# Kernel optimization log

Hardware: AMD Instinct MI355X
Metric: run time of the kernel (lower is better)

## Reference

```python
import jax, jax.numpy as jnp
import numpy as np

FEAT = 1152
HID = [768, 512, 256]
WS = 32
LN_EPS = 1e-5


def _ln(x, g, b):
    mu = jnp.mean(x, axis=-1, keepdims=True)
    var = jnp.mean(jnp.square(x - mu), axis=-1, keepdims=True)
    return (x - mu) * jax.lax.rsqrt(var + LN_EPS) * g + b


def setup_inputs() -> dict:
    key = jax.random.key(0)
    ks = jax.random.split(key, 16)
    B, N, C = 8, 9216, FEAT

    def lin(k, din, dout):
        s = 1.0 / np.sqrt(din)
        k1, k2 = jax.random.split(k)
        return (jax.random.uniform(k1, (din, dout), jnp.float32, -s, s),
                jax.random.uniform(k2, (dout,), jnp.float32, -s, s))

    x = jax.random.normal(ks[0], (B, N, C), jnp.float32)
    W1, b1 = lin(ks[1], C, HID[0])
    W2, b2 = lin(ks[2], HID[0], HID[1])
    W3, b3 = lin(ks[3], HID[1], HID[2])
    Wo, bo = lin(ks[4], HID[2], C)
    red = C // 8
    ca_w1, ca_b1 = lin(ks[5], C, red)
    ca_w2, ca_b2 = lin(ks[6], red, C)
    return {
        "x": x,
        "W1": W1, "b1": b1, "g1": jnp.ones((HID[0],)), "be1": jnp.zeros((HID[0],)),
        "W2": W2, "b2": b2, "g2": jnp.ones((HID[1],)), "be2": jnp.zeros((HID[1],)),
        "W3": W3, "b3": b3, "g3": jnp.ones((HID[2],)), "be3": jnp.zeros((HID[2],)),
        "Wo": Wo, "bo": bo,
        "ca_w1": ca_w1, "ca_b1": ca_b1, "ca_w2": ca_w2, "ca_b2": ca_b2,
    }


def reference(x, W1, b1, g1, be1, W2, b2, g2, be2, W3, b3, g3, be3,
              Wo, bo, ca_w1, ca_b1, ca_w2, ca_b2):
    B, N, C = x.shape
    # projection + hidden blocks: Linear -> GELU(exact) -> LayerNorm
    h = _ln(jax.nn.gelu(x @ W1 + b1, approximate=False), g1, be1)
    h = _ln(jax.nn.gelu(h @ W2 + b2, approximate=False), g2, be2)
    h = _ln(jax.nn.gelu(h @ W3 + b3, approximate=False), g3, be3)
    y = h @ Wo + bo  # (B, N, C)
    # SE channel attention: global avg-pool over seq, 1x1 convs (=linear)
    pooled = jnp.mean(y, axis=1)                                  # (B, C)
    s = jax.nn.relu(pooled @ ca_w1 + ca_b1)                       # (B, C/8)
    s = jax.nn.sigmoid(s @ ca_w2 + ca_b2)                         # (B, C)
    y = y * s[:, None, :]
    # block-diagonal local self-attention, window = WS, scale 1/sqrt(C)
    nw = N // WS
    yw = y.reshape(B, nw, WS, C)
    scores = jnp.einsum('bwqc,bwkc->bwqk', yw, yw) / jnp.sqrt(jnp.asarray(C, y.dtype))
    attn = jax.nn.softmax(scores, axis=-1)
    out = jnp.einsum('bwqk,bwkc->bwqc', attn, yw)
    return out.reshape(B, N, C)
```

## Files before the change

### kernel.cpp

```cpp
#include <hip/hip_runtime.h>
#include <cstdint>
#include <cstddef>

typedef __bf16 bf16;
typedef __bf16 bf16x8 __attribute__((ext_vector_type(8)));
typedef float f32x4 __attribute__((ext_vector_type(4)));

__device__ __forceinline__ void gload_lds16(const bf16* g, bf16* l) {
    __builtin_amdgcn_global_load_lds((const __attribute__((address_space(1))) void*)g,
                                     (__attribute__((address_space(3))) void*)l, 16, 0, 0);
}

__global__ void cvt_f32_bf16_kernel(const float* __restrict__ in, bf16* __restrict__ outp, size_t n) {
    const size_t i = ((size_t)blockIdx.x * 256 + threadIdx.x) * 8;
    if (i >= n) return;
    const float4 a = *(const float4*)(in + i);
    const float4 b = *(const float4*)(in + i + 4);
    bf16x8 o;
    o[0] = (bf16)a.x; o[1] = (bf16)a.y; o[2] = (bf16)a.z; o[3] = (bf16)a.w;
    o[4] = (bf16)b.x; o[5] = (bf16)b.y; o[6] = (bf16)b.z; o[7] = (bf16)b.w;
    *(bf16x8*)(outp + i) = o;
}

__global__ void wtrans_all_kernel(const float* __restrict__ W1, bf16* __restrict__ T1,
                                  const float* __restrict__ W2, bf16* __restrict__ T2,
                                  const float* __restrict__ W3, bf16* __restrict__ T3,
                                  const float* __restrict__ Wo, bf16* __restrict__ To)
{
    __shared__ bf16 tile[64][65];
    const int id = blockIdx.x;
    const int t = threadIdx.x;
    const float* W; bf16* T; int K, N, kb, nb;
    if (id < 216)      { W = W1; T = T1; K = 1152; N = 768;  const int r = id;       kb = r % 18; nb = r / 18; }
    else if (id < 312) { W = W2; T = T2; K = 768;  N = 512;  const int r = id - 216; kb = r % 12; nb = r / 12; }
    else if (id < 344) { W = W3; T = T3; K = 512;  N = 256;  const int r = id - 312; kb = r % 8;  nb = r / 8;  }
    else               { W = Wo; T = To; K = 256;  N = 1152; const int r = id - 344; kb = r % 4;  nb = r / 4;  }
    const int k0 = kb << 6;
    const int n0 = nb << 6;
#pragma unroll
    for (int i = 0; i < 16; ++i) {
        const int flat = i * 256 + t;
        const int r = flat >> 6;
        const int c = flat & 63;
        tile[c][r] = (bf16)W[(size_t)(k0 + r) * N + n0 + c];
    }
    __syncthreads();
#pragma unroll
    for (int i = 0; i < 16; ++i) {
        const int flat = i * 256 + t;
        const int r = flat >> 6;
        const int c = flat & 63;
        T[(size_t)(n0 + r) * K + k0 + c] = tile[r][c];
    }
}

__device__ __forceinline__ int xcd_swz(int bid, int nwg) {
    return (bid & 7) * (nwg >> 3) + (bid >> 3);
}

__global__ void gemm_bf16_kernel(const bf16* __restrict__ A, const bf16* __restrict__ Bt,
                                 const float* __restrict__ bias, bf16* __restrict__ C,
                                 int K, int N, int nx, int do_gelu)
{
    __shared__ bf16 Alds[128 * 64];
    __shared__ bf16 Blds[128 * 64];
    const int t = threadIdx.x;
    const int w = t >> 6;
    const int l = t & 63;
    const int l15 = l & 15, l4 = l >> 4;
    const int wgid = xcd_swz(blockIdx.x, gridDim.x);
    const int mblk = wgid / nx;
    const int nblk = wgid - mblk * nx;
    const int m0 = mblk << 7;
    const int n0 = nblk << 7;
    const int wm = (w >> 1) << 6;
    const int wn = (w & 1) << 6;

    f32x4 acc[4][4] = {};

    int sr[4], sg[4];
#pragma unroll
    for (int i = 0; i < 4; ++i) {
        const int flat = i * 256 + t;
        sr[i] = flat >> 3;
        sg[i] = ((flat & 7) ^ (sr[i] & 7)) << 3;
    }

    for (int k0 = 0; k0 < K; k0 += 64) {
#pragma unroll
        for (int i = 0; i < 4; ++i) {
            gload_lds16(A + (size_t)(m0 + sr[i]) * K + (k0 + sg[i]),
                        &Alds[(size_t)(i * 256 + (w << 6)) << 3]);
            gload_lds16(Bt + (size_t)(n0 + sr[i]) * K + (k0 + sg[i]),
                        &Blds[(size_t)(i * 256 + (w << 6)) << 3]);
        }
        __syncthreads();
#pragma unroll
        for (int kk = 0; kk < 2; ++kk) {
            bf16x8 af[4], bfv[4];
#pragma unroll
            for (int i = 0; i < 4; ++i) {
                const int r = wm + (i << 4) + l15;
                const int g = (kk << 2) + l4;
                af[i] = *(const bf16x8*)&Alds[(r << 6) + ((g ^ (r & 7)) << 3)];
                const int rn = wn + (i << 4) + l15;
                bfv[i] = *(const bf16x8*)&Blds[(rn << 6) + ((g ^ (rn & 7)) << 3)];
            }
#pragma unroll
            for (int i = 0; i < 4; ++i)
#pragma unroll
                for (int j = 0; j < 4; ++j)
                    acc[i][j] = __builtin_amdgcn_mfma_f32_16x16x32_bf16(af[i], bfv[j], acc[i][j], 0, 0, 0);
        }
        __syncthreads();
    }

#pragma unroll
    for (int i = 0; i < 4; ++i) {
        const int mb = m0 + wm + (i << 4) + (l4 << 2);
#pragma unroll
        for (int j = 0; j < 4; ++j) {
            const int col = n0 + wn + (j << 4) + l15;
            const float bv = bias[col];
#pragma unroll
            for (int r = 0; r < 4; ++r) {
                float v = acc[i][j][r] + bv;
                if (do_gelu) v = 0.5f * v * (1.0f + erff(v * 0.70710678118654752f));
                C[(size_t)(mb + r) * N + col] = (bf16)v;
            }
        }
    }
}

__global__ void ln768_kernel(bf16* __restrict__ H, const float* __restrict__ g,
                             const float* __restrict__ be)
{
    const int t = threadIdx.x;
    const int rloc = t >> 7;
    const int u = t & 127;
    bf16* hp = H + ((size_t)blockIdx.x * 2 + rloc) * 768;
    float v[8];
    float s1 = 0.f, s2 = 0.f;
    if (u < 96) {
        const bf16x8 hv = *(const bf16x8*)(hp + u * 8);
#pragma unroll
        for (int e = 0; e < 8; ++e) { v[e] = (float)hv[e]; s1 += v[e]; s2 += v[e] * v[e]; }
    }
#pragma unroll
    for (int m = 1; m < 64; m <<= 1) { s1 += __shfl_xor(s1, m, 64); s2 += __shfl_xor(s2, m, 64); }
    __shared__ float red[8];
    const int w = t >> 6;
    if ((t & 63) == 0) { red[w] = s1; red[w + 4] = s2; }
    __syncthreads();
    const int wb = rloc << 1;
    s1 = red[wb] + red[wb + 1];
    s2 = red[wb + 4] + red[wb + 5];
    const float mu = s1 * (1.0f / 768.0f);
    const float rstd = rsqrtf(s2 * (1.0f / 768.0f) - mu * mu + 1e-5f);
    if (u < 96) {
        const float4 g0 = *(const float4*)(g + u * 8);
        const float4 g1 = *(const float4*)(g + u * 8 + 4);
        const float4 b0 = *(const float4*)(be + u * 8);
        const float4 b1 = *(const float4*)(be + u * 8 + 4);
        bf16x8 o;
        o[0] = (bf16)((v[0] - mu) * rstd * g0.x + b0.x);
        o[1] = (bf16)((v[1] - mu) * rstd * g0.y + b0.y);
        o[2] = (bf16)((v[2] - mu) * rstd * g0.z + b0.z);
        o[3] = (bf16)((v[3] - mu) * rstd * g0.w + b0.w);
        o[4] = (bf16)((v[4] - mu) * rstd * g1.x + b1.x);
        o[5] = (bf16)((v[5] - mu) * rstd * g1.y + b1.y);
        o[6] = (bf16)((v[6] - mu) * rstd * g1.z + b1.z);
        o[7] = (bf16)((v[7] - mu) * rstd * g1.w + b1.w);
        *(bf16x8*)(hp + u * 8) = o;
    }
}

__global__ void ln512_kernel(bf16* __restrict__ H, const float* __restrict__ g,
                             const float* __restrict__ be)
{
    const int t = threadIdx.x;
    const int w = t >> 6, l = t & 63;
    bf16* hp = H + ((size_t)blockIdx.x * 4 + w) * 512;
    const bf16x8 hv = *(const bf16x8*)(hp + l * 8);
    float v[8];
    float s1 = 0.f, s2 = 0.f;
#pragma unroll
    for (int e = 0; e < 8; ++e) { v[e] = (float)hv[e]; s1 += v[e]; s2 += v[e] * v[e]; }
#pragma unroll
    for (int m = 1; m < 64; m <<= 1) { s1 += __shfl_xor(s1, m, 64); s2 += __shfl_xor(s2, m, 64); }
    const float mu = s1 * (1.0f / 512.0f);
    const float rstd = rsqrtf(s2 * (1.0f / 512.0f) - mu * mu + 1e-5f);
    const float4 g0 = *(const float4*)(g + l * 8);
    const float4 g1 = *(const float4*)(g + l * 8 + 4);
    const float4 b0 = *(const float4*)(be + l * 8);
    const float4 b1 = *(const float4*)(be + l * 8 + 4);
    bf16x8 o;
    o[0] = (bf16)((v[0] - mu) * rstd * g0.x + b0.x);
    o[1] = (bf16)((v[1] - mu) * rstd * g0.y + b0.y);
    o[2] = (bf16)((v[2] - mu) * rstd * g0.z + b0.z);
    o[3] = (bf16)((v[3] - mu) * rstd * g0.w + b0.w);
    o[4] = (bf16)((v[4] - mu) * rstd * g1.x + b1.x);
    o[5] = (bf16)((v[5] - mu) * rstd * g1.y + b1.y);
    o[6] = (bf16)((v[6] - mu) * rstd * g1.z + b1.z);
    o[7] = (bf16)((v[7] - mu) * rstd * g1.w + b1.w);
    *(bf16x8*)(hp + l * 8) = o;
}

__global__ void ln256_kernel(bf16* __restrict__ H, const float* __restrict__ g,
                             const float* __restrict__ be)
{
    const int t = threadIdx.x;
    const int rloc = t >> 5, l = t & 31;
    bf16* hp = H + ((size_t)blockIdx.x * 8 + rloc) * 256;
    const bf16x8 hv = *(const bf16x8*)(hp + l * 8);
    float v[8];
    float s1 = 0.f, s2 = 0.f;
#pragma unroll
    for (int e = 0; e < 8; ++e) { v[e] = (float)hv[e]; s1 += v[e]; s2 += v[e] * v[e]; }
#pragma unroll
    for (int m = 1; m < 32; m <<= 1) { s1 += __shfl_xor(s1, m, 64); s2 += __shfl_xor(s2, m, 64); }
    const float mu = s1 * (1.0f / 256.0f);
    const float rstd = rsqrtf(s2 * (1.0f / 256.0f) - mu * mu + 1e-5f);
    const float4 g0 = *(const float4*)(g + l * 8);
    const float4 g1 = *(const float4*)(g + l * 8 + 4);
    const float4 b0 = *(const float4*)(be + l * 8);
    const float4 b1 = *(const float4*)(be + l * 8 + 4);
    bf16x8 o;
    o[0] = (bf16)((v[0] - mu) * rstd * g0.x + b0.x);
    o[1] = (bf16)((v[1] - mu) * rstd * g0.y + b0.y);
    o[2] = (bf16)((v[2] - mu) * rstd * g0.z + b0.z);
    o[3] = (bf16)((v[3] - mu) * rstd * g0.w + b0.w);
    o[4] = (bf16)((v[4] - mu) * rstd * g1.x + b1.x);
    o[5] = (bf16)((v[5] - mu) * rstd * g1.y + b1.y);
    o[6] = (bf16)((v[6] - mu) * rstd * g1.z + b1.z);
    o[7] = (bf16)((v[7] - mu) * rstd * g1.w + b1.w);
    *(bf16x8*)(hp + l * 8) = o;
}

__global__ void pool1_kernel(const bf16* __restrict__ Y, float* __restrict__ ppart) {
    const int c = blockIdx.x * 128 + threadIdx.x;
    const int nc = blockIdx.y;
    const int b = blockIdx.z;
    const bf16* yp = Y + ((size_t)b * 9216 + (size_t)nc * 256) * 1152 + c;
    float s = 0.f;
#pragma unroll 4
    for (int i = 0; i < 256; ++i) s += (float)yp[(size_t)i * 1152];
    ppart[((size_t)b * 36 + nc) * 1152 + c] = s;
}

__global__ void se_kernel(const float* __restrict__ ppart,
                          const float* __restrict__ w1, const float* __restrict__ b1,
                          const float* __restrict__ w2, const float* __restrict__ b2,
                          float* __restrict__ sbuf)
{
    const int b = blockIdx.x, t = threadIdx.x;
    __shared__ float p[1152];
    __shared__ float t1[144];
    for (int c = t; c < 1152; c += 256) {
        float s = 0.f;
#pragma unroll
        for (int j = 0; j < 36; ++j) s += ppart[((size_t)b * 36 + j) * 1152 + c];
        p[c] = s * (1.0f / 9216.0f);
    }
    __syncthreads();
    if (t < 144) {
        float a = b1[t];
        for (int k = 0; k < 1152; ++k) a += p[k] * w1[k * 144 + t];
        t1[t] = a > 0.f ? a : 0.f;
    }
    __syncthreads();
    for (int c = t; c < 1152; c += 256) {
        float a = b2[c];
#pragma unroll 8
        for (int k = 0; k < 144; ++k) a += t1[k] * w2[k * 1152 + c];
        sbuf[b * 1152 + c] = 1.0f / (1.0f + expf(-a));
    }
}

__device__ __forceinline__ int fswz(int r) { return (r & 7) ^ ((r >> 3) & 3); }

__global__ void attn_kernel(const bf16* __restrict__ Y, const float* __restrict__ sbuf,
                            float* __restrict__ out)
{
    __shared__ bf16 yw[32 * 384];
    __shared__ float Sp[4][32][33];
    __shared__ bf16 P[32 * 32];

    const int t = threadIdx.x;
    const int w = t >> 6, l = t & 63;
    const int l15 = l & 15, l4 = l >> 4;
    const int wdx = blockIdx.x, b = blockIdx.y;

    const bf16* Yp = Y + ((size_t)b * 9216 + (size_t)wdx * 32) * 1152;
    const float* sv = sbuf + b * 1152;
    float* op = out + ((size_t)b * 9216 + (size_t)wdx * 32) * 1152;

    auto stage_chunk = [&](int cc) {
#pragma unroll
        for (int i = 0; i < 6; ++i) {
            const int flat = i * 256 + t;
            const int r = flat / 48;
            const int gg = flat - r * 48;
            const int c0 = cc * 384 + gg * 8;
            const bf16x8 yv = *(const bf16x8*)(Yp + (size_t)r * 1152 + c0);
            const float4 sa = *(const float4*)(sv + c0);
            const float4 sb = *(const float4*)(sv + c0 + 4);
            bf16x8 ov;
            ov[0] = (bf16)((float)yv[0] * sa.x);
            ov[1] = (bf16)((float)yv[1] * sa.y);
            ov[2] = (bf16)((float)yv[2] * sa.z);
            ov[3] = (bf16)((float)yv[3] * sa.w);
            ov[4] = (bf16)((float)yv[4] * sb.x);
            ov[5] = (bf16)((float)yv[5] * sb.y);
            ov[6] = (bf16)((float)yv[6] * sb.z);
            ov[7] = (bf16)((float)yv[7] * sb.w);
            *(bf16x8*)&yw[((r * 48) + (gg ^ fswz(r))) << 3] = ov;
        }
    };

    f32x4 acc[2][2] = {};
    for (int cc = 0; cc < 3; ++cc) {
        if (cc) __syncthreads();
        stage_chunk(cc);
        __syncthreads();
#pragma unroll
        for (int kkl = 0; kkl < 3; ++kkl) {
            const int g = ((w * 3 + kkl) << 2) + l4;
            bf16x8 af[2];
#pragma unroll
            for (int i = 0; i < 2; ++i) {
                const int r = (i << 4) + l15;
                af[i] = *(const bf16x8*)&yw[((r * 48) + (g ^ fswz(r))) << 3];
            }
#pragma unroll
            for (int i = 0; i < 2; ++i)
#pragma unroll
                for (int j = 0; j < 2; ++j)
                    acc[i][j] = __builtin_amdgcn_mfma_f32_16x16x32_bf16(af[i], af[j], acc[i][j], 0, 0, 0);
        }
    }
#pragma unroll
    for (int i = 0; i < 2; ++i)
#pragma unroll
        for (int j = 0; j < 2; ++j)
#pragma unroll
            for (int r = 0; r < 4; ++r)
                Sp[w][(i << 4) + (l4 << 2) + r][(j << 4) + l15] = acc[i][j][r];
    __syncthreads();

    {
        const int q = t >> 3, u = t & 7;
        float v[4];
#pragma unroll
        for (int e = 0; e < 4; ++e) {
            const int k2 = (u << 2) + e;
            v[e] = (Sp[0][q][k2] + Sp[1][q][k2] + Sp[2][q][k2] + Sp[3][q][k2]) * 0.029462782549439483f;
        }
        float mx = fmaxf(fmaxf(v[0], v[1]), fmaxf(v[2], v[3]));
#pragma unroll
        for (int m = 1; m < 8; m <<= 1) mx = fmaxf(mx, __shfl_xor(mx, m, 64));
        float sm = 0.f;
#pragma unroll
        for (int e = 0; e < 4; ++e) { v[e] = expf(v[e] - mx); sm += v[e]; }
#pragma unroll
        for (int m = 1; m < 8; m <<= 1) sm += __shfl_xor(sm, m, 64);
        const float inv = 1.0f / sm;
#pragma unroll
        for (int e = 0; e < 4; ++e) P[(q << 5) + (u << 2) + e] = (bf16)(v[e] * inv);
    }
    __syncthreads();

    bf16x8 pa[2];
#pragma unroll
    for (int i = 0; i < 2; ++i)
        pa[i] = *(const bf16x8*)&P[(((i << 4) + l15) << 5) + (l4 << 3)];

    for (int ci = 0; ci < 3; ++ci) {
        const int cc = (ci == 0) ? 2 : (ci - 1);
        if (ci) {
            __syncthreads();
            stage_chunk(cc);
            __syncthreads();
        }
        f32x4 pacc[2][6] = {};
#pragma unroll
        for (int jn = 0; jn < 6; ++jn) {
            const int nl = w * 96 + (jn << 4) + l15;
            const int gg = nl >> 3, e = nl & 7;
            bf16x8 bv;
#pragma unroll
            for (int j = 0; j < 8; ++j) {
                const int kr = (l4 << 3) + j;
                bv[j] = yw[(((kr * 48) + (gg ^ fswz(kr))) << 3) + e];
            }
#pragma unroll
            for (int i = 0; i < 2; ++i)
                pacc[i][jn] = __builtin_amdgcn_mfma_f32_16x16x32_bf16(pa[i], bv, pacc[i][jn], 0, 0, 0);
        }
#pragma unroll
        for (int i = 0; i < 2; ++i) {
            const int mb = (i << 4) + (l4 << 2);
#pragma unroll
            for (int jn = 0; jn < 6; ++jn) {
                const int cg = cc * 384 + w * 96 + (jn << 4) + l15;
#pragma unroll
                for (int r = 0; r < 4; ++r)
                    op[(size_t)(mb + r) * 1152 + cg] = pacc[i][jn][r];
            }
        }
    }
}

extern "C" void kernel_launch(void* const* d_in, const int* in_sizes, int n_in,
                              void* d_out, int out_size, void* d_ws, size_t ws_size,
                              hipStream_t stream)
{
    const float* x   = (const float*)d_in[0];
    const float* W1  = (const float*)d_in[1];
    const float* b1  = (const float*)d_in[2];
    const float* g1  = (const float*)d_in[3];
    const float* be1 = (const float*)d_in[4];
    const float* W2  = (const float*)d_in[5];
    const float* b2  = (const float*)d_in[6];
    const float* g2  = (const float*)d_in[7];
    const float* be2 = (const float*)d_in[8];
    const float* W3  = (const float*)d_in[9];
    const float* b3  = (const float*)d_in[10];
    const float* g3  = (const float*)d_in[11];
    const float* be3 = (const float*)d_in[12];
    const float* Wo  = (const float*)d_in[13];
    const float* bo  = (const float*)d_in[14];
    const float* cw1 = (const float*)d_in[15];
    const float* cb1 = (const float*)d_in[16];
    const float* cw2 = (const float*)d_in[17];
    const float* cb2 = (const float*)d_in[18];
    float* out = (float*)d_out;

    const int M = 8 * 9216;
    size_t off = 0;
    auto alloc = [&](size_t nbytes) {
        void* p = (char*)d_ws + off;
        off += (nbytes + 255) & ~(size_t)255;
        return p;
    };
    bf16* Yb  = (bf16*)alloc((size_t)M * 1152 * 2);
    bf16* Hb  = (bf16*)alloc((size_t)M * 768 * 2);
    bf16* H2  = (bf16*)alloc((size_t)M * 512 * 2);
    bf16* Wt1 = (bf16*)alloc(768ull * 1152 * 2);
    bf16* Wt2 = (bf16*)alloc(512ull * 768 * 2);
    bf16* Wt3 = (bf16*)alloc(256ull * 512 * 2);
    bf16* Wto = (bf16*)alloc(1152ull * 256 * 2);
    float* ppart = (float*)alloc(8ull * 36 * 1152 * 4);
    float* sbuf  = (float*)alloc(8ull * 1152 * 4);
    bf16* Xb = Yb;
    bf16* H1 = Hb;
    bf16* H3 = Hb;

    cvt_f32_bf16_kernel<<<41472, 256, 0, stream>>>(x, Xb, (size_t)M * 1152);
    wtrans_all_kernel<<<416, 256, 0, stream>>>(W1, Wt1, W2, Wt2, W3, Wt3, Wo, Wto);

    gemm_bf16_kernel<<<6 * 576, 256, 0, stream>>>(Xb, Wt1, b1, H1, 1152, 768, 6, 1);
    ln768_kernel<<<M / 2, 256, 0, stream>>>(H1, g1, be1);
    gemm_bf16_kernel<<<4 * 576, 256, 0, stream>>>(H1, Wt2, b2, H2, 768, 512, 4, 1);
    ln512_kernel<<<M / 4, 256, 0, stream>>>(H2, g2, be2);
    gemm_bf16_kernel<<<2 * 576, 256, 0, stream>>>(H2, Wt3, b3, H3, 512, 256, 2, 1);
    ln256_kernel<<<M / 8, 256, 0, stream>>>(H3, g3, be3);
    gemm_bf16_kernel<<<9 * 576, 256, 0, stream>>>(H3, Wto, bo, Yb, 256, 1152, 9, 0);

    pool1_kernel<<<dim3(9, 36, 8), 128, 0, stream>>>(Yb, ppart);
    se_kernel<<<8, 256, 0, stream>>>(ppart, cw1, cb1, cw2, cb2, sbuf);
    attn_kernel<<<dim3(288, 8), 256, 0, stream>>>(Yb, sbuf, out);
}
```

Before: 871.6 us.

## Replace GEMM with 256x128-tile, 512-thread, triple-buffered LDS pipelined kernel

The bf16 GEMM changes from 128x128 tiles with 256 threads to 256x128 tiles with 512 threads (8 waves). The K loop now triple-buffers LDS tiles, prefetching two steps ahead with global_load_lds, and interleaves those prefetches with MFMA groups under s_setprio. Synchronisation uses explicit vmcnt waits plus a single barrier per K step. The aim is to hide global-load latency and cut barrier stalls, in exchange for more LDS use (144KB per block), which limits occupancy.

```diff
diff --git a/kernel.cpp b/kernel.cpp
--- a/kernel.cpp
+++ b/kernel.cpp
@@ -58,69 +58,143 @@
     return (bid & 7) * (nwg >> 3) + (bid >> 3);
 }
 
-__global__ void gemm_bf16_kernel(const bf16* __restrict__ A, const bf16* __restrict__ Bt,
-                                 const float* __restrict__ bias, bf16* __restrict__ C,
-                                 int K, int N, int nx, int do_gelu)
-{
-    __shared__ bf16 Alds[128 * 64];
-    __shared__ bf16 Blds[128 * 64];
+__global__ __launch_bounds__(512, 2)
+void gemm_dp_kernel(const bf16* __restrict__ A, const bf16* __restrict__ Bt,
+                    const float* __restrict__ bias, bf16* __restrict__ C,
+                    int K, int N, int nx, int do_gelu)
+{
+    __shared__ bf16 lds[3 * 24576];
     const int t = threadIdx.x;
-    const int w = t >> 6;
-    const int l = t & 63;
+    const int w = t >> 6, l = t & 63;
     const int l15 = l & 15, l4 = l >> 4;
     const int wgid = xcd_swz(blockIdx.x, gridDim.x);
-    const int mblk = wgid / nx;
-    const int nblk = wgid - mblk * nx;
-    const int m0 = mblk << 7;
+    const int mblk = wgid / nx, nblk = wgid - mblk * nx;
+    const int m0 = mblk << 8;
     const int n0 = nblk << 7;
-    const int wm = (w >> 1) << 6;
-    const int wn = (w & 1) << 6;
+    const int wmB = (w >> 1) << 6;
+    const int wnB = (w & 1) << 6;
 
     f32x4 acc[4][4] = {};
 
-    int sr[4], sg[4];
+    int aRow[4], aCol[4];
 #pragma unroll
     for (int i = 0; i < 4; ++i) {
-        const int flat = i * 256 + t;
-        sr[i] = flat >> 3;
-        sg[i] = ((flat & 7) ^ (sr[i] & 7)) << 3;
-    }
-
-    for (int k0 = 0; k0 < K; k0 += 64) {
-#pragma unroll
-        for (int i = 0; i < 4; ++i) {
-            gload_lds16(A + (size_t)(m0 + sr[i]) * K + (k0 + sg[i]),
-                        &Alds[(size_t)(i * 256 + (w << 6)) << 3]);
-            gload_lds16(Bt + (size_t)(n0 + sr[i]) * K + (k0 + sg[i]),
-                        &Blds[(size_t)(i * 256 + (w << 6)) << 3]);
-        }
-        __syncthreads();
-#pragma unroll
-        for (int kk = 0; kk < 2; ++kk) {
-            bf16x8 af[4], bfv[4];
-#pragma unroll
-            for (int i = 0; i < 4; ++i) {
-                const int r = wm + (i << 4) + l15;
-                const int g = (kk << 2) + l4;
-                af[i] = *(const bf16x8*)&Alds[(r << 6) + ((g ^ (r & 7)) << 3)];
-                const int rn = wn + (i << 4) + l15;
-                bfv[i] = *(const bf16x8*)&Blds[(rn << 6) + ((g ^ (rn & 7)) << 3)];
-            }
-#pragma unroll
-            for (int i = 0; i < 4; ++i)
-#pragma unroll
-                for (int j = 0; j < 4; ++j)
-                    acc[i][j] = __builtin_amdgcn_mfma_f32_16x16x32_bf16(af[i], bfv[j], acc[i][j], 0, 0, 0);
-        }
-        __syncthreads();
+        const int flat = i * 512 + t;
+        aRow[i] = flat >> 3;
+        aCol[i] = ((flat & 7) ^ (aRow[i] & 7)) << 3;
+    }
+
+    const int NT = K >> 6;
+
+    auto stageA2 = [&](int kt, int ps, int i0) {
+#pragma unroll
+        for (int i2 = 0; i2 < 2; ++i2) {
+            const int i = i0 + i2;
+            gload_lds16(A + (size_t)(m0 + aRow[i]) * K + (kt << 6) + aCol[i],
+                        &lds[ps * 24576 + ((i * 512 + (w << 6)) << 3)]);
+        }
+    };
+    auto stageB2 = [&](int kt, int ps) {
+#pragma unroll
+        for (int i = 0; i < 2; ++i) {
+            gload_lds16(Bt + (size_t)(n0 + aRow[i]) * K + (kt << 6) + aCol[i],
+                        &lds[ps * 24576 + 16384 + ((i * 512 + (w << 6)) << 3)]);
+        }
+    };
+
+    stageA2(0, 0, 0); stageA2(0, 0, 2); stageB2(0, 0);
+    stageA2(1, 1, 0); stageA2(1, 1, 2); stageB2(1, 1);
+    asm volatile("s_waitcnt vmcnt(6)" ::: "memory");
+    __builtin_amdgcn_s_barrier();
+
+    int s = 0;
+    for (int kt = 0; kt < NT; ++kt) {
+        const int ps = (s == 0) ? 2 : s - 1;
+        const bool pf = (kt + 2) < NT;
+        const bf16* lA = &lds[s * 24576];
+        const bf16* lB = &lds[s * 24576 + 16384];
+
+        bf16x8 bfr[4], afr[2];
+
+#pragma unroll
+        for (int n = 0; n < 4; ++n) {
+            const int r = wnB + (n << 4) + l15;
+            bfr[n] = *(const bf16x8*)&lB[(r << 6) + ((l4 ^ (r & 7)) << 3)];
+        }
+#pragma unroll
+        for (int mi = 0; mi < 2; ++mi) {
+            const int r = wmB + (mi << 4) + l15;
+            afr[mi] = *(const bf16x8*)&lA[(r << 6) + ((l4 ^ (r & 7)) << 3)];
+        }
+        if (pf) stageA2(kt + 2, ps, 0);
+        __builtin_amdgcn_s_setprio(1);
+#pragma unroll
+        for (int mi = 0; mi < 2; ++mi)
+#pragma unroll
+            for (int n = 0; n < 4; ++n)
+                acc[mi][n] = __builtin_amdgcn_mfma_f32_16x16x32_bf16(afr[mi], bfr[n], acc[mi][n], 0, 0, 0);
+        __builtin_amdgcn_s_setprio(0);
+
+#pragma unroll
+        for (int mi = 0; mi < 2; ++mi) {
+            const int r = wmB + ((mi + 2) << 4) + l15;
+            afr[mi] = *(const bf16x8*)&lA[(r << 6) + ((l4 ^ (r & 7)) << 3)];
+        }
+        if (pf) stageA2(kt + 2, ps, 2);
+        __builtin_amdgcn_s_setprio(1);
+#pragma unroll
+        for (int mi = 0; mi < 2; ++mi)
+#pragma unroll
+            for (int n = 0; n < 4; ++n)
+                acc[mi + 2][n] = __builtin_amdgcn_mfma_f32_16x16x32_bf16(afr[mi], bfr[n], acc[mi + 2][n], 0, 0, 0);
+        __builtin_amdgcn_s_setprio(0);
+
+#pragma unroll
+        for (int n = 0; n < 4; ++n) {
+            const int r = wnB + (n << 4) + l15;
+            bfr[n] = *(const bf16x8*)&lB[(r << 6) + (((4 + l4) ^ (r & 7)) << 3)];
+        }
+#pragma unroll
+        for (int mi = 0; mi < 2; ++mi) {
+            const int r = wmB + (mi << 4) + l15;
+            afr[mi] = *(const bf16x8*)&lA[(r << 6) + (((4 + l4) ^ (r & 7)) << 3)];
+        }
+        if (pf) stageB2(kt + 2, ps);
+        __builtin_amdgcn_s_setprio(1);
+#pragma unroll
+        for (int mi = 0; mi < 2; ++mi)
+#pragma unroll
+            for (int n = 0; n < 4; ++n)
+                acc[mi][n] = __builtin_amdgcn_mfma_f32_16x16x32_bf16(afr[mi], bfr[n], acc[mi][n], 0, 0, 0);
+        __builtin_amdgcn_s_setprio(0);
+
+#pragma unroll
+        for (int mi = 0; mi < 2; ++mi) {
+            const int r = wmB + ((mi + 2) << 4) + l15;
+            afr[mi] = *(const bf16x8*)&lA[(r << 6) + (((4 + l4) ^ (r & 7)) << 3)];
+        }
+        __builtin_amdgcn_s_setprio(1);
+#pragma unroll
+        for (int mi = 0; mi < 2; ++mi)
+#pragma unroll
+            for (int n = 0; n < 4; ++n)
+                acc[mi + 2][n] = __builtin_amdgcn_mfma_f32_16x16x32_bf16(afr[mi], bfr[n], acc[mi + 2][n], 0, 0, 0);
+        __builtin_amdgcn_s_setprio(0);
+
+        if (kt + 1 < NT) {
+            if (pf) { asm volatile("s_waitcnt vmcnt(6)" ::: "memory"); }
+            else    { asm volatile("s_waitcnt vmcnt(0)" ::: "memory"); }
+            __builtin_amdgcn_s_barrier();
+        }
+        s = (s == 2) ? 0 : s + 1;
     }
 
 #pragma unroll
     for (int i = 0; i < 4; ++i) {
-        const int mb = m0 + wm + (i << 4) + (l4 << 2);
+        const int mb = m0 + wmB + (i << 4) + (l4 << 2);
 #pragma unroll
         for (int j = 0; j < 4; ++j) {
-            const int col = n0 + wn + (j << 4) + l15;
+            const int col = n0 + wnB + (j << 4) + l15;
             const float bv = bias[col];
 #pragma unroll
             for (int r = 0; r < 4; ++r) {
@@ -459,13 +533,13 @@
     cvt_f32_bf16_kernel<<<41472, 256, 0, stream>>>(x, Xb, (size_t)M * 1152);
     wtrans_all_kernel<<<416, 256, 0, stream>>>(W1, Wt1, W2, Wt2, W3, Wt3, Wo, Wto);
 
-    gemm_bf16_kernel<<<6 * 576, 256, 0, stream>>>(Xb, Wt1, b1, H1, 1152, 768, 6, 1);
+    gemm_dp_kernel<<<288 * 6, 512, 0, stream>>>(Xb, Wt1, b1, H1, 1152, 768, 6, 1);
     ln768_kernel<<<M / 2, 256, 0, stream>>>(H1, g1, be1);
-    gemm_bf16_kernel<<<4 * 576, 256, 0, stream>>>(H1, Wt2, b2, H2, 768, 512, 4, 1);
+    gemm_dp_kernel<<<288 * 4, 512, 0, stream>>>(H1, Wt2, b2, H2, 768, 512, 4, 1);
     ln512_kernel<<<M / 4, 256, 0, stream>>>(H2, g2, be2);
-    gemm_bf16_kernel<<<2 * 576, 256, 0, stream>>>(H2, Wt3, b3, H3, 512, 256, 2, 1);
+    gemm_dp_kernel<<<288 * 2, 512, 0, stream>>>(H2, Wt3, b3, H3, 512, 256, 2, 1);
     ln256_kernel<<<M / 8, 256, 0, stream>>>(H3, g3, be3);
-    gemm_bf16_kernel<<<9 * 576, 256, 0, stream>>>(H3, Wto, bo, Yb, 256, 1152, 9, 0);
+    gemm_dp_kernel<<<288 * 9, 512, 0, stream>>>(H3, Wto, bo, Yb, 256, 1152, 9, 0);
 
     pool1_kernel<<<dim3(9, 36, 8), 128, 0, stream>>>(Yb, ppart);
     se_kernel<<<8, 256, 0, stream>>>(ppart, cw1, cb1, cw2, cb2, sbuf);
```

Result: slower. 926.4 us (+6.3%).

## Add 256x256-tile 8-wave GEMM with phased LDS prefetch for hidden layers

Applied to the files above, without the earlier changes.

Adds a new 512-thread GEMM kernel that computes 256x256 output tiles. It splits each K-step into four MFMA phases, interleaves LDS fragment reads and async global-to-LDS prefetch two stages ahead between barriers, and raises wave priority during MFMA bursts. The first three projection GEMMs use it; the output GEMM keeps the old 128x128 kernel. Larger tiles cut global traffic per FLOP, at the cost of fewer workgroups (288 for the 256-wide layer, which may underfill the CUs), high register pressure and 128KB of LDS per block.

```diff
diff --git a/kernel.cpp b/kernel.cpp
--- a/kernel.cpp
+++ b/kernel.cpp
@@ -56,6 +56,150 @@
 
 __device__ __forceinline__ int xcd_swz(int bid, int nwg) {
     return (bid & 7) * (nwg >> 3) + (bid >> 3);
+}
+
+__global__ __launch_bounds__(512, 2)
+void gemm_8ph_kernel(const bf16* __restrict__ A, const bf16* __restrict__ Bt,
+                     const float* __restrict__ bias, bf16* __restrict__ C,
+                     int K, int N, int nx, int do_gelu)
+{
+    __shared__ bf16 lds[2 * 32768];
+    const int t = threadIdx.x;
+    const int w = t >> 6, l = t & 63;
+    const int l15 = l & 15, l4 = l >> 4;
+    const int wm = w >> 2, wn = w & 3;
+    const int wgid = xcd_swz(blockIdx.x, gridDim.x);
+    const int mblk = wgid / nx, nblk = wgid - mblk * nx;
+    const int m0 = mblk << 8, n0 = nblk << 8;
+
+    const int srow = t >> 3;
+    const int sgrp = (t & 7) ^ (srow & 7);
+    const int NT = K >> 6;
+
+    auto stageA = [&](int kt, int q) {
+        gload_lds16(A + (size_t)(m0 + (q << 6) + srow) * K + (kt << 6) + (sgrp << 3),
+                    &lds[((kt & 1) << 15) + (q << 12) + (w << 9)]);
+    };
+    auto stageB = [&](int kt, int q) {
+        gload_lds16(Bt + (size_t)(n0 + (q << 6) + srow) * K + (kt << 6) + (sgrp << 3),
+                    &lds[((kt & 1) << 15) + 16384 + (q << 12) + (w << 9)]);
+    };
+
+    f32x4 acc[8][4] = {};
+
+#pragma unroll
+    for (int q = 0; q < 4; ++q) stageA(0, q);
+#pragma unroll
+    for (int q = 0; q < 4; ++q) stageB(0, q);
+#pragma unroll
+    for (int q = 0; q < 4; ++q) stageA(1, q);
+#pragma unroll
+    for (int q = 0; q < 4; ++q) stageB(1, q);
+    asm volatile("s_waitcnt vmcnt(8)" ::: "memory");
+    __builtin_amdgcn_s_barrier();
+
+    for (int kt = 0; kt < NT; ++kt) {
+        const bf16* lA = &lds[(kt & 1) << 15];
+        const bf16* lB = lA + 16384;
+        const bool pf = (kt + 2) < NT;
+
+        bf16x8 aLo[8], aHi[8], bb[8];
+
+#pragma unroll
+        for (int i = 0; i < 4; ++i) {
+            const int r = (wm << 7) + (i << 4) + l15;
+            aLo[i]     = *(const bf16x8*)&lA[(r << 6) + ((l4 ^ (r & 7)) << 3)];
+            aLo[i + 4] = *(const bf16x8*)&lA[(r << 6) + (((4 + l4) ^ (r & 7)) << 3)];
+        }
+#pragma unroll
+        for (int j = 0; j < 2; ++j) {
+            const int r = (wn << 6) + (j << 4) + l15;
+            bb[j]     = *(const bf16x8*)&lB[(r << 6) + ((l4 ^ (r & 7)) << 3)];
+            bb[j + 2] = *(const bf16x8*)&lB[(r << 6) + (((4 + l4) ^ (r & 7)) << 3)];
+        }
+        __builtin_amdgcn_s_barrier();
+        __builtin_amdgcn_s_setprio(1);
+#pragma unroll
+        for (int i = 0; i < 4; ++i)
+#pragma unroll
+            for (int j = 0; j < 2; ++j) {
+                acc[i][j] = __builtin_amdgcn_mfma_f32_16x16x32_bf16(aLo[i], bb[j], acc[i][j], 0, 0, 0);
+                acc[i][j] = __builtin_amdgcn_mfma_f32_16x16x32_bf16(aLo[i + 4], bb[j + 2], acc[i][j], 0, 0, 0);
+            }
+        __builtin_amdgcn_s_setprio(0);
+        __builtin_amdgcn_s_barrier();
+
+#pragma unroll
+        for (int i = 0; i < 4; ++i) {
+            const int r = (wm << 7) + ((i + 4) << 4) + l15;
+            aHi[i]     = *(const bf16x8*)&lA[(r << 6) + ((l4 ^ (r & 7)) << 3)];
+            aHi[i + 4] = *(const bf16x8*)&lA[(r << 6) + (((4 + l4) ^ (r & 7)) << 3)];
+        }
+        if (pf) { stageA(kt + 2, 0); stageA(kt + 2, 2); }
+        __builtin_amdgcn_s_barrier();
+        __builtin_amdgcn_s_setprio(1);
+#pragma unroll
+        for (int i = 0; i < 4; ++i)
+#pragma unroll
+            for (int j = 0; j < 2; ++j) {
+                acc[i + 4][j] = __builtin_amdgcn_mfma_f32_16x16x32_bf16(aHi[i], bb[j], acc[i + 4][j], 0, 0, 0);
+                acc[i + 4][j] = __builtin_amdgcn_mfma_f32_16x16x32_bf16(aHi[i + 4], bb[j + 2], acc[i + 4][j], 0, 0, 0);
+            }
+        __builtin_amdgcn_s_setprio(0);
+        __builtin_amdgcn_s_barrier();
+
+#pragma unroll
+        for (int j = 0; j < 2; ++j) {
+            const int r = (wn << 6) + ((j + 2) << 4) + l15;
+            bb[j + 4] = *(const bf16x8*)&lB[(r << 6) + ((l4 ^ (r & 7)) << 3)];
+            bb[j + 6] = *(const bf16x8*)&lB[(r << 6) + (((4 + l4) ^ (r & 7)) << 3)];
+        }
+        if (pf) { stageA(kt + 2, 1); stageA(kt + 2, 3); }
+        __builtin_amdgcn_s_barrier();
+        __builtin_amdgcn_s_setprio(1);
+#pragma unroll
+        for (int i = 0; i < 4; ++i)
+#pragma unroll
+            for (int j = 0; j < 2; ++j) {
+                acc[i][j + 2] = __builtin_amdgcn_mfma_f32_16x16x32_bf16(aLo[i], bb[j + 4], acc[i][j + 2], 0, 0, 0);
+                acc[i][j + 2] = __builtin_amdgcn_mfma_f32_16x16x32_bf16(aLo[i + 4], bb[j + 6], acc[i][j + 2], 0, 0, 0);
+            }
+        __builtin_amdgcn_s_setprio(0);
+        __builtin_amdgcn_s_barrier();
+
+        if (pf) { stageB(kt + 2, 0); stageB(kt + 2, 1); stageB(kt + 2, 2); stageB(kt + 2, 3); }
+        __builtin_amdgcn_s_barrier();
+        __builtin_amdgcn_s_setprio(1);
+#pragma unroll
+        for (int i = 0; i < 4; ++i)
+#pragma unroll
+            for (int j = 0; j < 2; ++j) {
+                acc[i + 4][j + 2] = __builtin_amdgcn_mfma_f32_16x16x32_bf16(aHi[i], bb[j + 4], acc[i + 4][j + 2], 0, 0, 0);
+                acc[i + 4][j + 2] = __builtin_amdgcn_mfma_f32_16x16x32_bf16(aHi[i + 4], bb[j + 6], acc[i + 4][j + 2], 0, 0, 0);
+            }
+        __builtin_amdgcn_s_setprio(0);
+        if (kt + 1 < NT) {
+            if (pf) { asm volatile("s_waitcnt vmcnt(8)" ::: "memory"); }
+            else    { asm volatile("s_waitcnt vmcnt(0)" ::: "memory"); }
+            __builtin_amdgcn_s_barrier();
+        }
+    }
+
+#pragma unroll
+    for (int mi = 0; mi < 8; ++mi) {
+        const int mb = m0 + (wm << 7) + (mi << 4) + (l4 << 2);
+#pragma unroll
+        for (int ni = 0; ni < 4; ++ni) {
+            const int col = n0 + (wn << 6) + (ni << 4) + l15;
+            const float bv = bias[col];
+#pragma unroll
+            for (int r = 0; r < 4; ++r) {
+                float v = acc[mi][ni][r] + bv;
+                if (do_gelu) v = 0.5f * v * (1.0f + erff(v * 0.70710678118654752f));
+                C[(size_t)(mb + r) * N + col] = (bf16)v;
+            }
+        }
+    }
 }
 
 __global__ void gemm_bf16_kernel(const bf16* __restrict__ A, const bf16* __restrict__ Bt,
@@ -459,13 +603,13 @@
     cvt_f32_bf16_kernel<<<41472, 256, 0, stream>>>(x, Xb, (size_t)M * 1152);
     wtrans_all_kernel<<<416, 256, 0, stream>>>(W1, Wt1, W2, Wt2, W3, Wt3, Wo, Wto);
 
-    gemm_bf16_kernel<<<6 * 576, 256, 0, stream>>>(Xb, Wt1, b1, H1, 1152, 768, 6, 1);
+    gemm_8ph_kernel<<<288 * 3, 512, 0, stream>>>(Xb, Wt1, b1, H1, 1152, 768, 3, 1);
     ln768_kernel<<<M / 2, 256, 0, stream>>>(H1, g1, be1);
-    gemm_bf16_kernel<<<4 * 576, 256, 0, stream>>>(H1, Wt2, b2, H2, 768, 512, 4, 1);
+    gemm_8ph_kernel<<<288 * 2, 512, 0, stream>>>(H1, Wt2, b2, H2, 768, 512, 2, 1);
     ln512_kernel<<<M / 4, 256, 0, stream>>>(H2, g2, be2);
-    gemm_bf16_kernel<<<2 * 576, 256, 0, stream>>>(H2, Wt3, b3, H3, 512, 256, 2, 1);
+    gemm_8ph_kernel<<<288 * 1, 512, 0, stream>>>(H2, Wt3, b3, H3, 512, 256, 1, 1);
     ln256_kernel<<<M / 8, 256, 0, stream>>>(H3, g3, be3);
-    gemm_bf16_kernel<<<9 * 576, 256, 0, stream>>>(H3, Wto, bo, Yb, 256, 1152, 9, 0);
+    gemm_bf16_kernel<<<576 * 9, 256, 0, stream>>>(H3, Wto, bo, Yb, 256, 1152, 9, 0);
 
     pool1_kernel<<<dim3(9, 36, 8), 128, 0, stream>>>(Yb, ppart);
     se_kernel<<<8, 256, 0, stream>>>(ppart, cw1, cb1, cw2, cb2, sbuf);
```

New measurement: 987.0 us. 1.13x slower.
